# Optimization experiments

Measured on AMD Instinct MI355X. Metric: run time of the kernel, lower is better.

The kernel has to match this reference:

```python
import jax, jax.numpy as jnp
import numpy as np
import itertools

# ---- module constants (mirroring HyperLayer init) ----
B = 16          # batchsize
K = 16384       # number of learned index tuples (k)
ADD = 32        # additional sampled integer tuples per point
RANK = 2        # len(learn_cols) = w_rank; learn_cols = (0, 1)
P = 2 ** RANK + ADD  # candidate integer tuples per real-valued point
IN_DIM = 65536
OUT_DIM = 65536
EPSILON = 1e-6
SIGMA_BOOST = 2.0

# floor/ceil mask: rows of itertools.product([True, False], repeat=RANK) -> (2^RANK, RANK)
_FLOOR_MASK = jnp.array(
    [[int(b) for b in bools] for bools in itertools.product([True, False], repeat=RANK)],
    dtype=bool,
)


def setup_inputs() -> dict:
    key = jax.random.key(0)
    k1, k2, k3, k4 = jax.random.split(key, 4)
    return {
        "x": jax.random.normal(k1, (B, IN_DIM), jnp.float32),
        "res": jax.random.normal(k2, (B, K, RANK + 2), jnp.float32),
        "bias": jax.random.normal(k3, (OUT_DIM,), jnp.float32),
        "temp_indices": jax.random.randint(k4, (K, 2), 0, IN_DIM, dtype=jnp.int64),
    }


def _forward(x, res, bias, temp_indices):
    bsz = x.shape[0]
    # subrange = [out_size, in_size] for learn_cols = (0, 1)
    size = jnp.array([OUT_DIM, IN_DIM], jnp.float32)

    # ---- split_out: means in [0, size-1], sigmas softplus-scaled by size ----
    means = jax.nn.sigmoid(res[..., :RANK]) * (size - 1.0)               # (B, K, 2)
    sigmas = (jax.nn.softplus(res[..., RANK] + SIGMA_BOOST) + EPSILON)[..., None] * size  # (B, K, 2)
    values = res[..., RANK + 1]                                          # (B, K)

    # ---- discretize: 2^RANK floor/ceil neighbors (on detached means) ----
    m_det = jax.lax.stop_gradient(means)[:, :, None, :]                  # (B, K, 1, 2)
    nb = jnp.where(_FLOOR_MASK[None, None], jnp.floor(m_det), jnp.ceil(m_det)).astype(jnp.int32)  # (B,K,4,2)

    # additional uniformly sampled integer tuples (fixed internal key, deterministic)
    u = jax.random.uniform(jax.random.key(42), (bsz, K, ADD, RANK), jnp.float32) * (1.0 - EPSILON)
    samp = jnp.floor(u * size).astype(jnp.int32)                         # (B, K, ADD, 2)

    ints = jnp.concatenate([nb, samp], axis=2)                           # (B, K, P, 2)
    ints_fl = ints.astype(jnp.float32)

    # diagonal-Gaussian densities of integer tuples under (means, sigmas)
    z = (ints_fl - means[:, :, None, :]) / sigmas[:, :, None, :]         # (B, K, P, 2)
    props = jnp.exp(-0.5 * jnp.sum(z * z, axis=-1))                      # (B, K, P)
    props = props / jnp.sum(props + EPSILON, axis=2, keepdims=True)

    vals = (values[:, :, None] * props).reshape(bsz, -1)                 # (B, L)
    idx = ints.reshape(bsz, -1, RANK)                                    # (B, L, 2)

    # template: hardwired temp_indices, with learn_cols overwritten by discretized indices
    template = jnp.broadcast_to(
        temp_indices.astype(jnp.int32)[None, :, None, :], (bsz, K, P, 2)
    ).reshape(bsz, -1, 2)
    template = template.at[:, :, jnp.array([0, 1])].set(idx)

    out_idx = template[..., 0]                                           # (B, L) in [0, OUT_DIM)
    in_idx = template[..., 1]                                            # (B, L) in [0, IN_DIM)

    # sparse matrix-vector product per batch element: gather then scatter-add
    gathered = jnp.take_along_axis(x, in_idx, axis=1)                    # (B, L)
    contrib = vals * gathered                                            # (B, L)
    flat = (jnp.arange(bsz, dtype=jnp.int32)[:, None] * OUT_DIM + out_idx).reshape(-1)
    y = jnp.zeros((bsz * OUT_DIM,), x.dtype).at[flat].add(contrib.reshape(-1))
    return y.reshape(bsz, OUT_DIM) + bias[None, :]


def reference(x, res, bias, temp_indices):
    return _forward(x, res, bias, temp_indices)
```

## Files before the change

kernel.cpp:

```cpp
#include <hip/hip_runtime.h>
#include <stdint.h>
#include <math.h>

#define NB 16
#define NK 16384
#define NADD 32
#define NP 36
#define DIM 65536

#define TPB 512
#define GPB2 32
#define NCH3 4
#define CHW3 16384

typedef float f32x4 __attribute__((ext_vector_type(4)));
typedef unsigned int u32x2 __attribute__((ext_vector_type(2)));

__device__ __forceinline__ uint32_t rotl32(uint32_t x, uint32_t r) {
    return (x << r) | (x >> (32u - r));
}

__device__ __forceinline__ uint32_t tf_bits(uint32_t idx) {
    const uint32_t K1 = 42u;
    const uint32_t K2 = 0x1BD11BDAu ^ 42u;
    uint32_t x0 = 0u;
    uint32_t x1 = idx + K1;
#define TF_ROUND(r) { x0 += x1; x1 = rotl32(x1, r); x1 ^= x0; }
#define TF_G(a,b,c,d) TF_ROUND(a) TF_ROUND(b) TF_ROUND(c) TF_ROUND(d)
    TF_G(13,15,26,6)   x0 += K1;  x1 += K2 + 1u;
    TF_G(17,29,16,24)  x0 += K2;  x1 += 2u;
    TF_G(13,15,26,6)              x1 += K1 + 3u;
    TF_G(17,29,16,24)  x0 += K1;  x1 += K2 + 4u;
    TF_G(13,15,26,6)   x0 += K2;  x1 += 5u;
#undef TF_G
#undef TF_ROUND
    return x0 ^ x1;
}

__device__ __forceinline__ float xla_expf(float x0) {
    float x = fminf(fmaxf(x0, -88.3762626647949f), 88.3762626647950f);
    const float fx = floorf(__fadd_rn(__fmul_rn(x, 1.44269504088896341f), 0.5f));
    const float tmp = __fmul_rn(fx, 0.693359375f);
    float z = __fmul_rn(fx, -2.12194440e-4f);
    float r = __fsub_rn(x, tmp);
    r = __fsub_rn(r, z);
    z = __fmul_rn(r, r);
    float y = 1.9875691500E-4f;
    y = __fadd_rn(__fmul_rn(y, r), 1.3981999507E-3f);
    y = __fadd_rn(__fmul_rn(y, r), 8.3334519073E-3f);
    y = __fadd_rn(__fmul_rn(y, r), 4.1665795894E-2f);
    y = __fadd_rn(__fmul_rn(y, r), 1.6666665459E-1f);
    y = __fadd_rn(__fmul_rn(y, r), 5.0000001201E-1f);
    y = __fadd_rn(__fmul_rn(y, z), r);
    y = __fadd_rn(y, 1.0f);
    const int n = (int)fx;
    const float p2n = __uint_as_float((uint32_t)(n + 127) << 23);
    return fmaxf(__fmul_rn(y, p2n), x0);
}

__device__ __forceinline__ void gen_point(const float4 r, uint32_t tid,
                                          uint32_t* packed, float* w) {
    const float e0 = xla_expf(-r.x);
    const float e1 = xla_expf(-r.y);
    const float s0 = __fdiv_rn(1.0f, __fadd_rn(1.0f, e0));
    const float s1 = __fdiv_rn(1.0f, __fadd_rn(1.0f, e1));
    const float m0 = __fmul_rn(s0, 65535.0f);
    const float m1 = __fmul_rn(s1, 65535.0f);

    const float a2 = r.z + 2.0f;
    const float sp = fmaxf(a2, 0.0f) + log1pf(expf(-fabsf(a2)));
    const float sigma = (sp + 1e-6f) * 65536.0f;
    const float val = r.w;

    const float f0 = floorf(m0), c0 = ceilf(m0);
    const float f1 = floorf(m1), c1 = ceilf(m1);
    {
        const float cd0[4] = {f0, f0, c0, c0};
        const float cd1[4] = {f1, c1, f1, c1};
        #pragma unroll
        for (int p = 0; p < 4; ++p) {
            const float z0 = (cd0[p] - m0) / sigma;
            const float z1 = (cd1[p] - m1) / sigma;
            w[p] = expf(-0.5f * (z0*z0 + z1*z1));
            packed[p] = ((uint32_t)(int)cd0[p] << 16) | (uint32_t)(int)cd1[p];
        }
    }
    const float ONE_MEPS = (float)(1.0 - 1e-6);
    const uint32_t base = tid * 64u;
    #pragma unroll
    for (int a = 0; a < NADD; ++a) {
        const uint32_t bb0 = tf_bits(base + 2u*(uint32_t)a);
        const uint32_t bb1 = tf_bits(base + 2u*(uint32_t)a + 1u);
        const float u0 = __fmul_rn(__uint_as_float((bb0 >> 9) | 0x3f800000u) - 1.0f, ONE_MEPS);
        const float u1 = __fmul_rn(__uint_as_float((bb1 >> 9) | 0x3f800000u) - 1.0f, ONE_MEPS);
        const float s0f = floorf(__fmul_rn(u0, 65536.0f));
        const float s1f = floorf(__fmul_rn(u1, 65536.0f));
        const float z0 = (s0f - m0) / sigma;
        const float z1 = (s1f - m1) / sigma;
        w[4 + a] = expf(-0.5f * (z0*z0 + z1*z1));
        packed[4 + a] = ((uint32_t)(int)s0f << 16) | (uint32_t)(int)s1f;
    }
    float denom = 0.0f;
    #pragma unroll
    for (int p = 0; p < NP; ++p) denom += w[p] + 1e-6f;
    const float scale = val / denom;
    #pragma unroll
    for (int p = 0; p < NP; ++p) w[p] *= scale;
}

__device__ __forceinline__ uint32_t bf16pair(float a, float b) {
    uint32_t ua = __float_as_uint(a), ub = __float_as_uint(b);
    ua = (ua + 0x7FFFu + ((ua >> 16) & 1u)) >> 16;
    ub = (ub + 0x7FFFu + ((ub >> 16) & 1u)) >> 16;
    return ua | (ub << 16);
}


__global__ __launch_bounds__(TPB, 4) void f1_gen_reduce_bf16(
    const float*  __restrict__ x,
    const float4* __restrict__ res4,
    uint32_t* __restrict__ part)
{
    __shared__ float acc[CHW3];
    f32x4* const acc4 = reinterpret_cast<f32x4*>(acc);
    const int blk = blockIdx.x;
    const uint32_t tid = (uint32_t)blk * TPB + threadIdx.x;
    const int b = (int)(tid >> 14);

    uint32_t packed[NP];
    float    w[NP];
    gen_point(res4[tid], tid, packed, w);

    const float* __restrict__ xrow = x + ((size_t)b << 16);
    #pragma unroll
    for (int p = 0; p < NP; ++p) {
        w[p] *= xrow[packed[p] & 0xFFFFu];
        packed[p] = packed[p] >> 16;
    }

    #pragma unroll
    for (int j = 0; j < 8; ++j)
        acc4[j * TPB + threadIdx.x] = (f32x4)(0.0f);
    __syncthreads();

    uint32_t* __restrict__ dst = part + ((size_t)blk << 15);
    #pragma unroll 1
    for (uint32_t c = 0; c < NCH3; ++c) {
        #pragma unroll
        for (int p = 0; p < NP; ++p) {
            if ((packed[p] >> 14) == c)
                atomicAdd(&acc[packed[p] & (CHW3 - 1)], w[p]);
        }
        __syncthreads();
        u32x2* __restrict__ dst2 =
            reinterpret_cast<u32x2*>(dst + (size_t)c * 8192);
        #pragma unroll
        for (int j = 0; j < 8; ++j) {
            const int idx = j * TPB + (int)threadIdx.x;
            const f32x4 v = acc4[idx];
            const u32x2 o = { bf16pair(v.x, v.y), bf16pair(v.z, v.w) };
            __builtin_nontemporal_store(o, &dst2[idx]);
            acc4[idx] = (f32x4)(0.0f);
        }
        __syncthreads();
    }
}

__global__ __launch_bounds__(256) void f2_final_bf16(
    const u32x2* __restrict__ part2,
    const f32x4* __restrict__ bias4,
    f32x4* __restrict__ y4)
{
    const int i = blockIdx.x * 256 + threadIdx.x;
    const int o4 = i & 16383;
    const int b = i >> 14;
    f32x4 s = bias4[o4];
    #pragma unroll
    for (int g = 0; g < GPB2; ++g) {
        const u32x2 p = __builtin_nontemporal_load(
            &part2[(((size_t)(b * GPB2 + g)) << 14) + o4]);
        s.x += __uint_as_float(p.x << 16);
        s.y += __uint_as_float(p.x & 0xFFFF0000u);
        s.z += __uint_as_float(p.y << 16);
        s.w += __uint_as_float(p.y & 0xFFFF0000u);
    }
    __builtin_nontemporal_store(s, &y4[i]);
}


__global__ __launch_bounds__(256) void init_bias_kernel(
    const float4* __restrict__ bias4, float4* __restrict__ y4)
{
    const int i = blockIdx.x * 256 + threadIdx.x;
    y4[i] = bias4[i & 16383];
}

__global__ __launch_bounds__(256) void hyper_scatter(
    const float*  __restrict__ x,
    const float4* __restrict__ res4,
    float*        __restrict__ y)
{
    const int tid = blockIdx.x * 256 + threadIdx.x;
    const int b = tid >> 14;
    uint32_t packed[NP];
    float    w[NP];
    gen_point(res4[tid], (uint32_t)tid, packed, w);
    const float* __restrict__ xrow = x + ((size_t)b << 16);
    float*       __restrict__ yrow = y + ((size_t)b << 16);
    #pragma unroll
    for (int p = 0; p < NP; ++p) {
        const float xv = xrow[packed[p] & 0xFFFFu];
        unsafeAtomicAdd(&yrow[packed[p] >> 16], w[p] * xv);
    }
}

extern "C" void kernel_launch(void* const* d_in, const int* in_sizes, int n_in,
                              void* d_out, int out_size, void* d_ws, size_t ws_size,
                              hipStream_t stream) {
    const float*  x     = (const float*)d_in[0];
    const float4* res4  = (const float4*)d_in[1];
    const float4* bias4 = (const float4*)d_in[2];
    float* y = (float*)d_out;

    const size_t need_bf16 = (size_t)NB * GPB2 * DIM * 2;

    if (ws_size >= need_bf16) {
        uint32_t* part = (uint32_t*)d_ws;
        f1_gen_reduce_bf16<<<NB * GPB2, TPB, 0, stream>>>(x, res4, part);
        f2_final_bf16<<<(NB * DIM / 4) / 256, 256, 0, stream>>>(
            (const u32x2*)part, (const f32x4*)bias4, (f32x4*)y);
    } else {
        init_bias_kernel<<<(NB * DIM / 4) / 256, 256, 0, stream>>>(bias4, (float4*)y);
        hyper_scatter<<<(NB * NK) / 256, 256, 0, stream>>>(x, res4, y);
    }
}
```

Baseline: 161.9 us.

## Use fast exp/rcp math, lighter barriers, and wider bf16 partial loads in reduce

Replaces per-candidate divisions by sigma with a single reciprocal and a precomputed -0.5/sigma² factor, and uses fast __expf instead of expf. Swaps __syncthreads for an explicit lgkmcnt wait plus s_barrier, and drops nontemporal hints on the partial-sum stores so they stay cacheable for the second kernel. The final reduction kernel now reads 16-byte bf16 chunks and writes 8 floats per thread, halving its thread count. Fast exp and rcp can perturb weights slightly against the reference, and the hand-written barrier only waits on LDS traffic.

```diff
diff --git a/kernel.cpp b/kernel.cpp
--- a/kernel.cpp
+++ b/kernel.cpp
@@ -14,7 +14,11 @@
 #define CHW3 16384
 
 typedef float f32x4 __attribute__((ext_vector_type(4)));
+typedef float f32x8 __attribute__((ext_vector_type(8)));
 typedef unsigned int u32x2 __attribute__((ext_vector_type(2)));
+typedef unsigned int u32x4 __attribute__((ext_vector_type(4)));
+
+#define BAR_LGKM() asm volatile("s_waitcnt lgkmcnt(0)\n\ts_barrier" ::: "memory")
 
 __device__ __forceinline__ uint32_t rotl32(uint32_t x, uint32_t r) {
     return (x << r) | (x >> (32u - r));
@@ -68,8 +72,10 @@
     const float m1 = __fmul_rn(s1, 65535.0f);
 
     const float a2 = r.z + 2.0f;
-    const float sp = fmaxf(a2, 0.0f) + log1pf(expf(-fabsf(a2)));
+    const float sp = fmaxf(a2, 0.0f) + log1pf(__expf(-fabsf(a2)));
     const float sigma = (sp + 1e-6f) * 65536.0f;
+    const float inv_sig = __builtin_amdgcn_rcpf(sigma);
+    const float n2 = -0.5f * inv_sig * inv_sig;
     const float val = r.w;
 
     const float f0 = floorf(m0), c0 = ceilf(m0);
@@ -79,9 +85,9 @@
         const float cd1[4] = {f1, c1, f1, c1};
         #pragma unroll
         for (int p = 0; p < 4; ++p) {
-            const float z0 = (cd0[p] - m0) / sigma;
-            const float z1 = (cd1[p] - m1) / sigma;
-            w[p] = expf(-0.5f * (z0*z0 + z1*z1));
+            const float d0 = cd0[p] - m0;
+            const float d1 = cd1[p] - m1;
+            w[p] = __expf(n2 * fmaf(d1, d1, d0 * d0));
             packed[p] = ((uint32_t)(int)cd0[p] << 16) | (uint32_t)(int)cd1[p];
         }
     }
@@ -95,15 +101,15 @@
         const float u1 = __fmul_rn(__uint_as_float((bb1 >> 9) | 0x3f800000u) - 1.0f, ONE_MEPS);
         const float s0f = floorf(__fmul_rn(u0, 65536.0f));
         const float s1f = floorf(__fmul_rn(u1, 65536.0f));
-        const float z0 = (s0f - m0) / sigma;
-        const float z1 = (s1f - m1) / sigma;
-        w[4 + a] = expf(-0.5f * (z0*z0 + z1*z1));
+        const float d0 = s0f - m0;
+        const float d1 = s1f - m1;
+        w[4 + a] = __expf(n2 * fmaf(d1, d1, d0 * d0));
         packed[4 + a] = ((uint32_t)(int)s0f << 16) | (uint32_t)(int)s1f;
     }
     float denom = 0.0f;
     #pragma unroll
     for (int p = 0; p < NP; ++p) denom += w[p] + 1e-6f;
-    const float scale = val / denom;
+    const float scale = __fdiv_rn(val, denom);
     #pragma unroll
     for (int p = 0; p < NP; ++p) w[p] *= scale;
 }
@@ -151,7 +157,7 @@
             if ((packed[p] >> 14) == c)
                 atomicAdd(&acc[packed[p] & (CHW3 - 1)], w[p]);
         }
-        __syncthreads();
+        BAR_LGKM();
         u32x2* __restrict__ dst2 =
             reinterpret_cast<u32x2*>(dst + (size_t)c * 8192);
         #pragma unroll
@@ -159,32 +165,35 @@
             const int idx = j * TPB + (int)threadIdx.x;
             const f32x4 v = acc4[idx];
             const u32x2 o = { bf16pair(v.x, v.y), bf16pair(v.z, v.w) };
-            __builtin_nontemporal_store(o, &dst2[idx]);
+            dst2[idx] = o;
             acc4[idx] = (f32x4)(0.0f);
         }
-        __syncthreads();
+        BAR_LGKM();
     }
 }
 
 __global__ __launch_bounds__(256) void f2_final_bf16(
-    const u32x2* __restrict__ part2,
-    const f32x4* __restrict__ bias4,
-    f32x4* __restrict__ y4)
+    const u32x4* __restrict__ part4,
+    const f32x8* __restrict__ bias8,
+    f32x8* __restrict__ y8)
 {
     const int i = blockIdx.x * 256 + threadIdx.x;
-    const int o4 = i & 16383;
-    const int b = i >> 14;
-    f32x4 s = bias4[o4];
+    const int o8 = i & 8191;
+    const int b = i >> 13;
+    f32x8 s = bias8[o8];
     #pragma unroll
     for (int g = 0; g < GPB2; ++g) {
-        const u32x2 p = __builtin_nontemporal_load(
-            &part2[(((size_t)(b * GPB2 + g)) << 14) + o4]);
-        s.x += __uint_as_float(p.x << 16);
-        s.y += __uint_as_float(p.x & 0xFFFF0000u);
-        s.z += __uint_as_float(p.y << 16);
-        s.w += __uint_as_float(p.y & 0xFFFF0000u);
-    }
-    __builtin_nontemporal_store(s, &y4[i]);
+        const u32x4 p = part4[(((size_t)(b * GPB2 + g)) << 13) + o8];
+        s[0] += __uint_as_float(p.x << 16);
+        s[1] += __uint_as_float(p.x & 0xFFFF0000u);
+        s[2] += __uint_as_float(p.y << 16);
+        s[3] += __uint_as_float(p.y & 0xFFFF0000u);
+        s[4] += __uint_as_float(p.z << 16);
+        s[5] += __uint_as_float(p.z & 0xFFFF0000u);
+        s[6] += __uint_as_float(p.w << 16);
+        s[7] += __uint_as_float(p.w & 0xFFFF0000u);
+    }
+    __builtin_nontemporal_store(s, &y8[i]);
 }
 
 
@@ -227,8 +236,8 @@
     if (ws_size >= need_bf16) {
         uint32_t* part = (uint32_t*)d_ws;
         f1_gen_reduce_bf16<<<NB * GPB2, TPB, 0, stream>>>(x, res4, part);
-        f2_final_bf16<<<(NB * DIM / 4) / 256, 256, 0, stream>>>(
-            (const u32x2*)part, (const f32x4*)bias4, (f32x4*)y);
+        f2_final_bf16<<<(NB * DIM / 8) / 256, 256, 0, stream>>>(
+            (const u32x4*)part, (const f32x8*)bias4, (f32x8*)y);
     } else {
         init_bias_kernel<<<(NB * DIM / 4) / 256, 256, 0, stream>>>(bias4, (float4*)y);
         hyper_scatter<<<(NB * NK) / 256, 256, 0, stream>>>(x, res4, y);
```

Result: no change. 160.1 us (-1.2%).
